# Performance work log

Measured on AMD Instinct MI355X. Metric: run time of the kernel, lower is better.

The kernel has to match this reference:

```python
import jax, jax.numpy as jnp
import numpy as np
import math

N, DIM, HEADS = 4096, 128, 8
HC = DIM // HEADS      # MHA per-head dim = 16
GC = DIM               # TransformerConv per-head out_channels = dim (concat=False)
E = 65536
FFN = 2048
EPS = 1e-5

def layernorm(x, g, b):
    m = x.mean(-1, keepdims=True)
    v = ((x - m) ** 2).mean(-1, keepdims=True)
    return (x - m) * jax.lax.rsqrt(v + EPS) * g + b

def setup_inputs() -> dict:
    key = jax.random.key(0)
    ks = jax.random.split(key, 24)
    s = 0.02
    def nrm(k, shape):
        return jax.random.normal(k, shape, jnp.float32) * s
    return dict(
        x=jax.random.normal(ks[0], (N, DIM), jnp.float32),
        edge_index=jax.random.randint(ks[1], (2, E), 0, N),
        edge_attr=jax.random.normal(ks[2], (E, DIM), jnp.float32),
        n1_g=jnp.ones((DIM,)), n1_b=jnp.zeros((DIM,)),
        n2_g=jnp.ones((DIM,)), n2_b=jnp.zeros((DIM,)),
        n3_g=jnp.ones((DIM,)), n3_b=jnp.zeros((DIM,)),
        w_qkv=nrm(ks[3], (DIM, 3 * DIM)), b_qkv=jnp.zeros((3 * DIM,)),
        w_o=nrm(ks[4], (DIM, DIM)), b_o=jnp.zeros((DIM,)),
        w_query=nrm(ks[5], (DIM, HEADS * GC)), b_query=jnp.zeros((HEADS * GC,)),
        w_key=nrm(ks[6], (DIM, HEADS * GC)), b_key=jnp.zeros((HEADS * GC,)),
        w_value=nrm(ks[7], (DIM, HEADS * GC)), b_value=jnp.zeros((HEADS * GC,)),
        w_edge=nrm(ks[8], (DIM, HEADS * GC)), b_edge=jnp.zeros((HEADS * GC,)),
        w_skip=nrm(ks[9], (DIM, GC)), b_skip=jnp.zeros((GC,)),
        w_beta=nrm(ks[10], (3 * GC, 1)),
        w_f1=nrm(ks[11], (DIM, FFN)), b_f1=jnp.zeros((FFN,)),
        w_f2=nrm(ks[12], (FFN, DIM)), b_f2=jnp.zeros((DIM,)),
        w_dyn=nrm(ks[13], (2 * DIM, DIM)), b_dyn=jnp.zeros((DIM,)),
    )

def reference(x, edge_index, edge_attr, n1_g, n1_b, n2_g, n2_b, n3_g, n3_b,
              w_qkv, b_qkv, w_o, b_o,
              w_query, b_query, w_key, b_key, w_value, b_value,
              w_edge, b_edge, w_skip, b_skip, w_beta,
              w_f1, b_f1, w_f2, b_f2, w_dyn, b_dyn):
    residual = x
    xn = layernorm(x, n1_g, n1_b)
    # ---- dense self-attention (batch 1, batch_first MHA, eval mode) ----
    qkv = xn @ w_qkv + b_qkv
    q, k, v = jnp.split(qkv, 3, axis=-1)
    q = q.reshape(N, HEADS, HC)
    k = k.reshape(N, HEADS, HC)
    v = v.reshape(N, HEADS, HC)
    scores = jnp.einsum('qhd,khd->hqk', q, k) / math.sqrt(HC)
    probs = jax.nn.softmax(scores, axis=-1)
    attn = jnp.einsum('hqk,khd->qhd', probs, v).reshape(N, DIM)
    attn = attn @ w_o + b_o
    x = residual + attn
    # ---- TransformerConv (heads=8, concat=False -> mean, beta=True, edge_dim=dim) ----
    xn2 = layernorm(x, n2_g, n2_b)
    src, dst = edge_index[0], edge_index[1]   # source -> target flow
    qg = (xn2 @ w_query + b_query).reshape(N, HEADS, GC)
    kg = (xn2 @ w_key + b_key).reshape(N, HEADS, GC)
    vg = (xn2 @ w_value + b_value).reshape(N, HEADS, GC)
    eg = (edge_attr @ w_edge + b_edge).reshape(E, HEADS, GC)
    kj = kg[src] + eg                          # key_j + edge embedding
    alpha = jnp.einsum('ehd,ehd->eh', qg[dst], kj) / math.sqrt(GC)  # [E,H]
    amax = jax.ops.segment_max(alpha, dst, num_segments=N)          # [N,H]
    amax = jnp.where(jnp.isfinite(amax), amax, 0.0)
    ea = jnp.exp(alpha - amax[dst])
    denom = jax.ops.segment_sum(ea, dst, num_segments=N)
    w = ea / (denom[dst] + 1e-16)              # segment softmax per target node
    msg = (vg[src] + eg) * w[:, :, None]       # value_j + edge, scaled
    agg = jax.ops.segment_sum(msg, dst, num_segments=N)  # [N,H,GC]
    out = agg.mean(axis=1)                     # concat=False -> head mean
    x_r = xn2 @ w_skip + b_skip                # root/skip path
    beta = jax.nn.sigmoid(jnp.concatenate([out, x_r, out - x_r], axis=-1) @ w_beta)
    graph_out = beta * x_r + (1.0 - beta) * out
    x = x + graph_out
    # ---- FFN ----
    xn3 = layernorm(x, n3_g, n3_b)
    ffn = jax.nn.gelu(xn3 @ w_f1 + b_f1, approximate=False) @ w_f2 + b_f2
    x = x + ffn
    # ---- gated residual fusion ----
    gate = jax.nn.sigmoid(jnp.concatenate([x, residual], axis=-1) @ w_dyn + b_dyn)
    return x * gate + residual * (1.0 - gate)
```

## Files before the change

kernel.cpp:

```cpp
#include <hip/hip_runtime.h>
#include <math.h>
#include <cstddef>

#define NN 4096
#define DIMC 128
#define NHEADS 8
#define NE 65536

typedef unsigned short ushort_t;
typedef short bs8 __attribute__((ext_vector_type(8)));
typedef float f32x16 __attribute__((ext_vector_type(16)));
typedef _Float16 h4 __attribute__((ext_vector_type(4)));
typedef float f4t __attribute__((ext_vector_type(4)));

__device__ __forceinline__ float b2f(ushort_t u){
  unsigned int i = ((unsigned int)u)<<16; float f;
  __builtin_memcpy(&f,&i,4); return f;
}
__device__ __forceinline__ ushort_t f2b(float f){
  unsigned int x; __builtin_memcpy(&x,&f,4);
  unsigned int r = x + 0x7fffu + ((x>>16)&1u);
  return (ushort_t)(r>>16);
}
__device__ __forceinline__ float bdot8(uint4 a, uint4 b){
  unsigned int ua[4]={a.x,a.y,a.z,a.w}, ub[4]={b.x,b.y,b.z,b.w};
  float s=0.f;
  #pragma unroll
  for (int i=0;i<4;++i){
    unsigned int al=ua[i]<<16, ah=ua[i]&0xffff0000u, bl=ub[i]<<16, bh=ub[i]&0xffff0000u;
    float fa,fb,fc,fd;
    __builtin_memcpy(&fa,&al,4); __builtin_memcpy(&fb,&ah,4);
    __builtin_memcpy(&fc,&bl,4); __builtin_memcpy(&fd,&bh,4);
    s += fa*fc + fb*fd;
  }
  return s;
}
__device__ __forceinline__ float bfdot8v(uint4 a, float4 e0, float4 e1){
  unsigned int ua[4]={a.x,a.y,a.z,a.w};
  float eb[8]={e0.x,e0.y,e0.z,e0.w,e1.x,e1.y,e1.z,e1.w};
  float s=0.f;
  #pragma unroll
  for (int i=0;i<4;++i){
    unsigned int al=ua[i]<<16, ah=ua[i]&0xffff0000u;
    float fa,fb;
    __builtin_memcpy(&fa,&al,4); __builtin_memcpy(&fb,&ah,4);
    s += fa*eb[2*i] + fb*eb[2*i+1];
  }
  return s;
}

__global__ __launch_bounds__(128) void ln_kernel(const float* __restrict__ x,
    const float* __restrict__ g, const float* __restrict__ b, ushort_t* __restrict__ y){
  int n = blockIdx.x, d = threadIdx.x;
  __shared__ float red[128];
  float v = x[(size_t)n*DIMC + d];
  red[d] = v; __syncthreads();
  for (int off=64; off>0; off>>=1){ if (d<off) red[d]+=red[d+off]; __syncthreads(); }
  float mean = red[0]*(1.0f/128.0f);
  __syncthreads();
  float c = v-mean;
  red[d] = c*c; __syncthreads();
  for (int off=64; off>0; off>>=1){ if (d<off) red[d]+=red[d+off]; __syncthreads(); }
  float var = red[0]*(1.0f/128.0f);
  y[(size_t)n*DIMC+d] = f2b(c*rsqrtf(var+1e-5f)*g[d]+b[d]);
}

#define QSCALE 0.36067376022224085f
__global__ __launch_bounds__(256) void megawcvt_kernel(
    const float* __restrict__ w_qkv, const float* __restrict__ w_o,
    const float* __restrict__ w_q, const float* __restrict__ w_k,
    const float* __restrict__ w_v, const float* __restrict__ w_e,
    const float* __restrict__ w_f1, const float* __restrict__ w_f2,
    const float* __restrict__ bq, const float* __restrict__ bk,
    const float* __restrict__ w_dyn, const float* __restrict__ b_qkv,
    ushort_t* __restrict__ WBqkv, ushort_t* __restrict__ WBo, ushort_t* __restrict__ WBG,
    ushort_t* __restrict__ WETB, ushort_t* __restrict__ WBf1, ushort_t* __restrict__ WBf2,
    ushort_t* __restrict__ WCAT, float* __restrict__ BCAT, ushort_t* __restrict__ WDYN,
    int* __restrict__ COUNT, float* __restrict__ BQKV)
{
  for (int id = blockIdx.x*256+threadIdx.x; id < 1284480; id += gridDim.x*256){
    if (id < 1245184){
      float v; ushort_t* dst; int local;
      if (id < 49152){ local=id; int n=local>>7,k=local&127; v=w_qkv[(size_t)k*384+n];
        if (n<128) v *= QSCALE;
        dst=&WBqkv[local]; }
      else if (id < 65536){ local=id-49152; int n=local>>7,k=local&127; v=w_o[(size_t)k*128+n]; dst=&WBo[local]; }
      else if (id < 327680){ local=id-65536; int n=local>>7,k=local&127;
        v = (n<1024) ? w_q[(size_t)k*1024+n] : w_k[(size_t)k*1024+n-1024];
        dst=&WBG[local]; }
      else if (id < 458752){ local=id-327680; int n=local>>7,k=local&127; v=w_e[(size_t)k*1024+n]; dst=&WETB[local]; }
      else if (id < 720896){ local=id-458752; int n=local>>7,k=local&127; v=w_f1[(size_t)k*2048+n]; dst=&WBf1[local]; }
      else if (id < 983040){ local=id-720896; int n=local>>11,k=local&2047; v=w_f2[(size_t)k*128+n]; dst=&WBf2[local]; }
      else { local=id-983040; int d=local>>11, k=local&2047;
        int h=(k&1023)>>7, i=k&127;
        const float* src = (k<1024) ? w_v : w_e;
        v = src[(size_t)i*1024 + h*128 + d]*0.125f;
        dst=&WCAT[local]; }
      *dst = f2b(v);
    } else if (id < 1247232){
      int local = id - 1245184;
      BCAT[local] = (local<1024) ? bq[local] : bk[local-1024];
    } else if (id < 1280000){
      int local = id - 1247232;
      WDYN[local] = f2b(w_dyn[local]);
    } else if (id < 1284096){
      COUNT[id-1280000]=0;
    } else {
      int local = id - 1284096;
      BQKV[local] = b_qkv[local] * ((local<128) ? QSCALE : 1.0f);
    }
  }
}

template<int A_BF16, int C_MODE>
__global__ __launch_bounds__(256) void mgemm_kernel(
    const void* __restrict__ Av, int lda, int strideA,
    const ushort_t* __restrict__ BT, int ldbt, int strideB,
    const float* __restrict__ bias,
    const float* __restrict__ res,
    void* __restrict__ Cv, int ldc, int strideC,
    int K, int act_gelu)
{
  int z = blockIdx.z;
  int m0 = blockIdx.y*128, n0 = blockIdx.x*64;
  int tid = threadIdx.x;
  int w = tid>>6, lane = tid&63;
  int kg = lane>>5;
  int ml = w*32 + (lane&31);
  int sw = (ml>>1)&3;
  __shared__ ushort_t As[128*32];
  const ushort_t* BTz = BT + (size_t)z*strideB;
  f32x16 acc[2];
  #pragma unroll
  for (int i=0;i<16;++i){ acc[0][i]=0.f; acc[1][i]=0.f; }

  for (int k0=0; k0<K; k0+=32){
    {
      int rr = tid>>1, kc = (tid&1)*16;
      int rowg = m0 + rr;
      ushort_t tmp[16] __attribute__((aligned(16)));
      if (A_BF16){
        const ushort_t* A = (const ushort_t*)Av + (size_t)z*strideA;
        uint4 u0 = *(const uint4*)&A[(size_t)rowg*lda + k0 + kc];
        uint4 u1 = *(const uint4*)&A[(size_t)rowg*lda + k0 + kc + 8];
        __builtin_memcpy(tmp, &u0, 16); __builtin_memcpy(tmp+8, &u1, 16);
      } else {
        const float* A = (const float*)Av + (size_t)z*strideA;
        const float* p = &A[(size_t)rowg*lda + k0 + kc];
        float4 f0=*(const float4*)p, f1=*(const float4*)(p+4);
        float4 f2v=*(const float4*)(p+8), f3=*(const float4*)(p+12);
        tmp[0]=f2b(f0.x); tmp[1]=f2b(f0.y); tmp[2]=f2b(f0.z); tmp[3]=f2b(f0.w);
        tmp[4]=f2b(f1.x); tmp[5]=f2b(f1.y); tmp[6]=f2b(f1.z); tmp[7]=f2b(f1.w);
        tmp[8]=f2b(f2v.x); tmp[9]=f2b(f2v.y); tmp[10]=f2b(f2v.z); tmp[11]=f2b(f2v.w);
        tmp[12]=f2b(f3.x); tmp[13]=f2b(f3.y); tmp[14]=f2b(f3.z); tmp[15]=f2b(f3.w);
      }
      int swr = (rr>>1)&3, c0 = kc>>3;
      *(uint4*)&As[rr*32 + (((c0  )^swr)*8)] = *(const uint4*)tmp;
      *(uint4*)&As[rr*32 + (((c0+1)^swr)*8)] = *(const uint4*)(tmp+8);
    }
    __syncthreads();
    bs8 a0 = *(bs8*)&As[ml*32 + (((0*2+kg)^sw)*8)];
    bs8 a1 = *(bs8*)&As[ml*32 + (((1*2+kg)^sw)*8)];
    #pragma unroll
    for (int nt=0; nt<2; ++nt){
      const ushort_t* bp = &BTz[(size_t)(n0 + nt*32 + (lane&31))*ldbt + k0 + kg*8];
      uint4 rb0 = *(const uint4*)bp;
      uint4 rb1 = *(const uint4*)(bp + 16);
      bs8 b0, b1;
      __builtin_memcpy(&b0, &rb0, 16); __builtin_memcpy(&b1, &rb1, 16);
      acc[nt] = __builtin_amdgcn_mfma_f32_32x32x16_bf16(a0, b0, acc[nt], 0,0,0);
      acc[nt] = __builtin_amdgcn_mfma_f32_32x32x16_bf16(a1, b1, acc[nt], 0,0,0);
    }
    __syncthreads();
  }
  #pragma unroll
  for (int nt=0; nt<2; ++nt){
    int col = n0 + nt*32 + (lane&31);
    float bv = bias ? bias[col] : 0.f;
    #pragma unroll
    for (int r=0; r<16; ++r){
      int rowl = (r&3) + 8*(r>>2) + 4*kg;
      int row = m0 + w*32 + rowl;
      float v = acc[nt][r] + bv;
      if (act_gelu) v = 0.5f*v*(1.0f+erff(v*0.70710678118654752f));
      if (res) v += res[(size_t)row*ldc + col];
      size_t idx = (size_t)z*strideC + (size_t)row*ldc + col;
      if (C_MODE==1)      ((ushort_t*)Cv)[idx] = f2b(v);
      else if (C_MODE==2) ((_Float16*)Cv)[idx] = (_Float16)v;
      else                ((float*)Cv)[idx]    = v;
    }
  }
}

__global__ __launch_bounds__(256) void vtrans_kernel(const _Float16* __restrict__ qkvh,
    _Float16* __restrict__ vt){
  int id = blockIdx.x*256+threadIdx.x;
  int n = id & 4095, d = id >> 12;
  vt[(size_t)d*4096 + n] = qkvh[(size_t)n*384 + 256 + d];
}

__global__ __launch_bounds__(512) void flash_kernel(const _Float16* __restrict__ qkvh,
    const _Float16* __restrict__ vt, float* __restrict__ attn){
  int h = blockIdx.y;
  int w = threadIdx.x >> 6, lane = threadIdx.x & 63;
  int q0 = blockIdx.x*64;
  int col = lane & 15, quad = lane >> 4;
  __shared__ float ll[8][4][16];
  __shared__ float lo[8][4][256];
  h4 qf[4];
  #pragma unroll
  for (int t=0;t<4;++t)
    qf[t] = *(const h4*)&qkvh[(size_t)(q0+t*16+col)*384 + h*16 + quad*4];
  f4t ov[4];
  float ls[4] = {0.f,0.f,0.f,0.f};
  #pragma unroll
  for (int t=0;t<4;++t){ ov[t][0]=0.f; ov[t][1]=0.f; ov[t][2]=0.f; ov[t][3]=0.f; }
  const _Float16* kbase = qkvh + 128 + h*16 + quad*4;
  const _Float16* vbase = vt + (size_t)(h*16+col)*4096 + quad*4;
  int jbeg = w*512, jend = jbeg + 512;
  h4 kf = *(const h4*)&kbase[(size_t)(jbeg+col)*384];
  h4 vf = *(const h4*)&vbase[jbeg];
  for (int j0=jbeg; j0<jend; j0+=16){
    h4 kc=kf, vc=vf;
    if (j0+16<jend){
      kf = *(const h4*)&kbase[(size_t)(j0+16+col)*384];
      vf = *(const h4*)&vbase[j0+16];
    }
    f4t s[4];
    #pragma unroll
    for (int t=0;t<4;++t){
      s[t][0]=0.f; s[t][1]=0.f; s[t][2]=0.f; s[t][3]=0.f;
      s[t] = __builtin_amdgcn_mfma_f32_16x16x16f16(kc, qf[t], s[t], 0,0,0);
    }
    #pragma unroll
    for (int t=0;t<4;++t){
      float p0=__builtin_amdgcn_exp2f(s[t][0]), p1=__builtin_amdgcn_exp2f(s[t][1]);
      float p2=__builtin_amdgcn_exp2f(s[t][2]), p3=__builtin_amdgcn_exp2f(s[t][3]);
      ls[t] += (p0+p1)+(p2+p3);
      h4 pf; pf[0]=(_Float16)p0; pf[1]=(_Float16)p1; pf[2]=(_Float16)p2; pf[3]=(_Float16)p3;
      ov[t] = __builtin_amdgcn_mfma_f32_16x16x16f16(vc, pf, ov[t], 0,0,0);
    }
  }
  #pragma unroll
  for (int t=0;t<4;++t){
    float l = ls[t];
    l += __shfl_xor(l,16);
    l += __shfl_xor(l,32);
    if (lane<16) ll[w][t][lane]=l;
    *(float4*)&lo[w][t][lane*4] = make_float4(ov[t][0],ov[t][1],ov[t][2],ov[t][3]);
  }
  __syncthreads();
  if (w < 4){
    int t = w;
    float l = 0.f;
    #pragma unroll
    for (int ww=0; ww<8; ++ww) l += ll[ww][t][col];
    float4 os = make_float4(0.f,0.f,0.f,0.f);
    #pragma unroll
    for (int ww=0; ww<8; ++ww){
      float4 owv = *(const float4*)&lo[ww][t][lane*4];
      os.x += owv.x; os.y += owv.y; os.z += owv.z; os.w += owv.w;
    }
    float inv = 1.0f/l;
    *(float4*)&attn[(size_t)(q0+t*16+col)*128 + h*16 + quad*4] =
        make_float4(os.x*inv, os.y*inv, os.z*inv, os.w*inv);
  }
}

__global__ __launch_bounds__(256) void alpha_kernel(
    const float* __restrict__ ea, const ushort_t* __restrict__ qkvsg,
    const ushort_t* __restrict__ t, const int* __restrict__ csr,
    const int* __restrict__ pack, float* __restrict__ alpha){
  int tid = threadIdx.x;
  int w = tid>>6, lane = tid&63;
  int h = lane>>3, li = lane&7;
  int off = h*128 + li*16;
  int ibase = blockIdx.x*8 + w*2;
  int2 pk = *(const int2*)&pack[ibase];
  int2 ec = *(const int2*)&csr[ibase];
  int e0 = ec.x & (NE-1), e1 = ec.y & (NE-1);
  int s0 = pk.x & 4095, d0 = (pk.x>>12) & 4095;
  int s1 = pk.y & 4095, d1 = (pk.y>>12) & 4095;

  const ushort_t* q0p = &qkvsg[(size_t)d0*2048 + off];
  const ushort_t* k0p = &qkvsg[(size_t)s0*2048 + 1024 + off];
  const ushort_t* t0p = &t[(size_t)d0*1024 + off];
  const float*    e0p = &ea[(size_t)e0*128 + li*16];
  const ushort_t* q1p = &qkvsg[(size_t)d1*2048 + off];
  const ushort_t* k1p = &qkvsg[(size_t)s1*2048 + 1024 + off];
  const ushort_t* t1p = &t[(size_t)d1*1024 + off];
  const float*    e1p = &ea[(size_t)e1*128 + li*16];

  uint4 q00=*(const uint4*)q0p,      q01=*(const uint4*)(q0p+8);
  uint4 k00=*(const uint4*)k0p,      k01=*(const uint4*)(k0p+8);
  uint4 t00=*(const uint4*)t0p,      t01=*(const uint4*)(t0p+8);
  float4 ea00=*(const float4*)e0p,   ea01=*(const float4*)(e0p+4);
  float4 ea02=*(const float4*)(e0p+8), ea03=*(const float4*)(e0p+12);
  uint4 q10=*(const uint4*)q1p,      q11=*(const uint4*)(q1p+8);
  uint4 k10=*(const uint4*)k1p,      k11=*(const uint4*)(k1p+8);
  uint4 t10=*(const uint4*)t1p,      t11=*(const uint4*)(t1p+8);
  float4 ea10=*(const float4*)e1p,   ea11=*(const float4*)(e1p+4);
  float4 ea12=*(const float4*)(e1p+8), ea13=*(const float4*)(e1p+12);

  float p0 = bdot8(q00,k00) + bdot8(q01,k01)
           + bfdot8v(t00,ea00,ea01) + bfdot8v(t01,ea02,ea03);
  float p1 = bdot8(q10,k10) + bdot8(q11,k11)
           + bfdot8v(t10,ea10,ea11) + bfdot8v(t11,ea12,ea13);
  p0 += __shfl_xor(p0,1); p0 += __shfl_xor(p0,2); p0 += __shfl_xor(p0,4);
  p1 += __shfl_xor(p1,1); p1 += __shfl_xor(p1,2); p1 += __shfl_xor(p1,4);
  if (li==0){
    alpha[(size_t)ibase*8 + h]     = 0.08838834764831845f*p0;
    alpha[(size_t)(ibase+1)*8 + h] = 0.08838834764831845f*p1;
  }
}

__global__ __launch_bounds__(256) void count_kernel(const int* __restrict__ ei, int* __restrict__ cnt){
  int e = blockIdx.x*256+threadIdx.x;
  atomicAdd(&cnt[ei[NE+e] & (NN-1)],1);
}
__global__ __launch_bounds__(1024) void scan_kernel(const int* __restrict__ cnt,
    int* __restrict__ rows, int* __restrict__ cursor){
  __shared__ int sums[1024];
  int tid=threadIdx.x;
  int c0=cnt[tid*4], c1=cnt[tid*4+1], c2=cnt[tid*4+2], c3=cnt[tid*4+3];
  int local=c0+c1+c2+c3;
  sums[tid]=local;
  __syncthreads();
  for (int off=1; off<1024; off<<=1){
    int v = (tid>=off)? sums[tid-off] : 0;
    __syncthreads();
    sums[tid]+=v;
    __syncthreads();
  }
  int r = sums[tid]-local;
  rows[tid*4]=r;   cursor[tid*4]=r;   r+=c0;
  rows[tid*4+1]=r; cursor[tid*4+1]=r; r+=c1;
  rows[tid*4+2]=r; cursor[tid*4+2]=r; r+=c2;
  rows[tid*4+3]=r; cursor[tid*4+3]=r; r+=c3;
  if (tid==1023) rows[4096]=r;
}
__global__ __launch_bounds__(256) void scatter_kernel(const int* __restrict__ ei,
    int* __restrict__ cursor, int* __restrict__ csr, int* __restrict__ pack){
  int e = blockIdx.x*256+threadIdx.x;
  int src = ei[e] & (NN-1), dst = ei[NE+e] & (NN-1);
  int pos = atomicAdd(&cursor[dst],1);
  if (pos >= 0 && pos < NE){ csr[pos]=e; pack[pos] = src | (dst<<12); }
}

__global__ __launch_bounds__(256) void agg1_kernel(
    const ushort_t* __restrict__ lns, const float* __restrict__ ea,
    const float* __restrict__ abuf, const int* __restrict__ rows, const int* __restrict__ csr,
    const int* __restrict__ pack,
    const float* __restrict__ b_edge, const float* __restrict__ b_v,
    ushort_t* __restrict__ seagg, float* __restrict__ part)
{
  int n = blockIdx.x, tid = threadIdx.x;
  int d = tid & 127, h0 = tid >> 7;
  float sacc[4]={0.f,0.f,0.f,0.f}, eacc[4]={0.f,0.f,0.f,0.f}, wsacc[4]={0.f,0.f,0.f,0.f};
  float mh[4]={-1e30f,-1e30f,-1e30f,-1e30f};
  float be[4];
  #pragma unroll
  for (int j=0;j<4;++j){
    int hd = (h0+2*j)*128 + d;
    be[j] = b_edge[hd] + b_v[hd];
  }
  int i0=rows[n], i1=rows[n+1];
  i0 = max(0,min(i0,NE)); i1 = max(i0,min(i1,NE));
  for (int i=i0;i<i1;++i){
    #pragma unroll
    for (int j=0;j<4;++j) mh[j] = fmaxf(mh[j], abuf[(size_t)i*8 + h0 + 2*j]);
  }
  __shared__ float smh[8];
  __shared__ float wls[16][8];
  __shared__ int es[16], srcs[16];
  if (d==0){
    #pragma unroll
    for (int j=0;j<4;++j) smh[h0+2*j]=mh[j];
  }
  __syncthreads();
  for (int cs=i0; cs<i1; cs+=16){
    int cnt = min(16, i1-cs);
    if (tid < cnt){
      es[tid]   = csr[cs+tid] & (NE-1);
      srcs[tid] = pack[cs+tid] & (NN-1);
    }
    if (tid < cnt*8){
      int k=tid>>3, hh=tid&7;
      wls[k][hh] = __expf(abuf[(size_t)(cs+k)*8+hh]-smh[hh]);
    }
    __syncthreads();
    for (int k=0;k<cnt;++k){
      int e = es[k], sr = srcs[k];
      float lv = b2f(lns[(size_t)sr*128 + d]);
      float eav = ea[(size_t)e*128 + d];
      #pragma unroll
      for (int j=0;j<4;++j){
        float wv = wls[k][h0+2*j];
        sacc[j] += wv*lv;
        eacc[j] += wv*eav;
        wsacc[j] += wv;
      }
    }
    __syncthreads();
  }
  float partial = 0.f;
  #pragma unroll
  for (int j=0;j<4;++j){
    float inv = 1.0f/(wsacc[j]+1e-16f);
    int hd = (h0+2*j)*128 + d;
    seagg[(size_t)n*2048 + hd]        = f2b(sacc[j]*inv);
    seagg[(size_t)n*2048 + 1024 + hd] = f2b(eacc[j]*inv);
    partial += be[j]*wsacc[j]*inv;
  }
  __shared__ float pp[2][128];
  pp[h0][d] = partial;
  __syncthreads();
  if (tid<128) part[(size_t)n*128+tid] = (pp[0][tid]+pp[1][tid])*0.125f;
}

__global__ __launch_bounds__(128) void combine_kernel(float* __restrict__ x2,
    const float* __restrict__ corrp, const float* __restrict__ part,
    const ushort_t* __restrict__ lns, const float* __restrict__ w_s,
    const float* __restrict__ b_s, const float* __restrict__ x1,
    const float* __restrict__ w_beta)
{
  int n=blockIdx.x, d=threadIdx.x;
  __shared__ float lnrow[128];
  __shared__ float sred[128];
  __shared__ float sbeta;
  size_t idx = (size_t)n*128+d;
  lnrow[d] = b2f(lns[idx]);
  __syncthreads();
  float xrv = b_s[d];
  #pragma unroll 4
  for (int i=0;i<128;++i) xrv += lnrow[i]*w_s[(size_t)i*128+d];
  float o = part[idx] + corrp[idx] + corrp[524288+idx] + corrp[1048576+idx] + corrp[1572864+idx];
  sred[d] = o*w_beta[d] + xrv*w_beta[128+d] + (o-xrv)*w_beta[256+d];
  __syncthreads();
  for (int off=64; off>0; off>>=1){ if (d<off) sred[d]+=sred[d+off]; __syncthreads(); }
  if (d==0) sbeta = 1.0f/(1.0f+__expf(-sred[0]));
  __syncthreads();
  float beta=sbeta;
  x2[idx] = x1[idx] + beta*xrv + (1.0f-beta)*o;
}

__global__ __launch_bounds__(128) void gate_kernel(const float* __restrict__ x3p,
    const float* __restrict__ b_f2, const float* __restrict__ x2,
    const float* __restrict__ x0, const ushort_t* __restrict__ wdyn,
    const float* __restrict__ b_dyn, float* __restrict__ out){
  int n=blockIdx.x, d=threadIdx.x;
  __shared__ float s[256];
  size_t idx = (size_t)n*128+d;
  float a = x3p[idx] + x3p[524288+idx] + x3p[1048576+idx] + x3p[1572864+idx]
          + b_f2[d] + x2[idx];
  float r = x0[idx];
  s[d]=a; s[128+d]=r;
  __syncthreads();
  float g = b_dyn[d];
  for (int k=0;k<256;++k) g += s[k]*b2f(wdyn[(size_t)k*128+d]);
  g = 1.0f/(1.0f+__expf(-g));
  out[idx] = a*g + r*(1.0f-g);
}

extern "C" void kernel_launch(void* const* d_in, const int* in_sizes, int n_in,
                              void* d_out, int out_size, void* d_ws, size_t ws_size,
                              hipStream_t stream) {
  const float* x    =(const float*)d_in[0];
  const int*   ei   =(const int*)  d_in[1];
  const float* eattr=(const float*)d_in[2];
  const float* n1g=(const float*)d_in[3], *n1b=(const float*)d_in[4];
  const float* n2g=(const float*)d_in[5], *n2b=(const float*)d_in[6];
  const float* n3g=(const float*)d_in[7], *n3b=(const float*)d_in[8];
  const float* w_qkv=(const float*)d_in[9],  *b_qkv=(const float*)d_in[10];
  const float* w_o  =(const float*)d_in[11], *b_o  =(const float*)d_in[12];
  const float* w_q  =(const float*)d_in[13], *b_q  =(const float*)d_in[14];
  const float* w_k  =(const float*)d_in[15], *b_k  =(const float*)d_in[16];
  const float* w_v  =(const float*)d_in[17], *b_v  =(const float*)d_in[18];
  const float* w_e  =(const float*)d_in[19], *b_e  =(const float*)d_in[20];
  const float* w_s  =(const float*)d_in[21], *b_s  =(const float*)d_in[22];
  const float* w_beta=(const float*)d_in[23];
  const float* w_f1 =(const float*)d_in[24], *b_f1=(const float*)d_in[25];
  const float* w_f2 =(const float*)d_in[26], *b_f2=(const float*)d_in[27];
  const float* w_dyn=(const float*)d_in[28], *b_dyn=(const float*)d_in[29];
  float* out=(float*)d_out;
  float* ws=(float*)d_ws;

  float* X1    = ws + 0;
  float* X2    = ws + 524288;
  ushort_t* LNS = (ushort_t*)(ws + 1048576);
  float* PART  = ws + 1310720;
  float* ALPHA = ws + 1835008;
  int*   ROWS  = (int*)(ws + 2359296);
  int*   CURS  = (int*)(ws + 2363456);
  int*   CSR   = (int*)(ws + 2367552);
  int*   COUNT = (int*)(ws + 2433088);
  int*   PACK  = (int*)(ws + 524288);
  float* BQKV  = ws + 1048576 - 512;
  ushort_t* WBqkv = (ushort_t*)(ws + 2437184);
  ushort_t* WBo   = (ushort_t*)(ws + 2461760);
  ushort_t* WBG   = (ushort_t*)(ws + 2469952);
  ushort_t* WETB  = (ushort_t*)(ws + 2601024);
  ushort_t* WBf1  = (ushort_t*)(ws + 2666560);
  ushort_t* WBf2  = (ushort_t*)(ws + 2797632);
  ushort_t* WCAT  = (ushort_t*)(ws + 2928704);
  float* BCAT  = ws + 3059776;
  ushort_t* WDYN = (ushort_t*)(ws + 3061824);
  _Float16* QKVH  = (_Float16*)(ws + 3078208);
  _Float16* VT    = (_Float16*)(ws + 3864640);
  ushort_t* QKVSG = (ushort_t*)(ws + 3078208);
  ushort_t* SEAGG = (ushort_t*)(ws + 3078208);
  ushort_t* MID   = (ushort_t*)(ws + 3078208);
  ushort_t* T     = (ushort_t*)(ws + 7272512);
  float* CORRP = ws + 7272512;
  float* X3P   = ws + 7272512;
  float* ATTN  = X2;

  megawcvt_kernel<<<2048,256,0,stream>>>(w_qkv,w_o,w_q,w_k,w_v,w_e,w_f1,w_f2,
                                         b_q,b_k,w_dyn,b_qkv,
                                         WBqkv,WBo,WBG,WETB,WBf1,WBf2,WCAT,BCAT,WDYN,COUNT,BQKV);

  ln_kernel<<<NN,128,0,stream>>>(x, n1g, n1b, LNS);
  mgemm_kernel<1,2><<<dim3(6,32,1),256,0,stream>>>(LNS,128,0, WBqkv,128,0, BQKV, nullptr, QKVH,384,0, 128, 0);
  vtrans_kernel<<<2048,256,0,stream>>>(QKVH, VT);
  flash_kernel<<<dim3(64,8),512,0,stream>>>(QKVH, VT, ATTN);
  mgemm_kernel<0,0><<<dim3(2,32,1),256,0,stream>>>(ATTN,128,0, WBo,128,0, b_o, x, X1,128,0, 128, 0);

  ln_kernel<<<NN,128,0,stream>>>(X1, n2g, n2b, LNS);
  mgemm_kernel<1,1><<<dim3(32,32,1),256,0,stream>>>(LNS,128,0, WBG,128,0, BCAT, nullptr, QKVSG,2048,0, 128, 0);
  mgemm_kernel<1,1><<<dim3(2,32,8),256,0,stream>>>(QKVSG,2048,128, WETB,128,16384, nullptr, nullptr, T,1024,128, 128, 0);
  count_kernel<<<256,256,0,stream>>>(ei, COUNT);
  scan_kernel<<<1,1024,0,stream>>>(COUNT, ROWS, CURS);
  scatter_kernel<<<256,256,0,stream>>>(ei, CURS, CSR, PACK);
  alpha_kernel<<<8192,256,0,stream>>>(eattr, QKVSG, T, CSR, PACK, ALPHA);
  agg1_kernel<<<NN,256,0,stream>>>(LNS, eattr, ALPHA, ROWS, CSR, PACK, b_e, b_v, SEAGG, PART);
  mgemm_kernel<1,0><<<dim3(2,32,4),256,0,stream>>>(SEAGG,2048,512, WCAT,2048,512, nullptr, nullptr, CORRP,128,524288, 512, 0);
  combine_kernel<<<NN,128,0,stream>>>(X2, CORRP, PART, LNS, w_s, b_s, X1, w_beta);

  ln_kernel<<<NN,128,0,stream>>>(X2, n3g, n3b, LNS);
  mgemm_kernel<1,1><<<dim3(32,32,1),256,0,stream>>>(LNS,128,0, WBf1,128,0, b_f1, nullptr, MID,2048,0, 128, 1);
  mgemm_kernel<1,0><<<dim3(2,32,4),256,0,stream>>>(MID,2048,512, WBf2,2048,512, nullptr, nullptr, X3P,128,524288, 512, 0);

  gate_kernel<<<NN,128,0,stream>>>(X3P, b_f2, X2, x, WDYN, b_dyn, out);
}
```

Before: 399.2 us.

## Use wave-level layernorm, fuse V transpose and third layernorm, rework combine/gate kernels

Rewrites the layernorm kernel to do one row per wavefront with shuffle reductions and paired loads. The V transpose moves into the QKV GEMM epilogue, and the third layernorm is fused into combine_kernel, removing two launches and their extra memory passes. Combine and gate kernels now process two rows per 64-thread block with float2 accesses, so each weight load is reused across two rows. Flash attention uses packed round-toward-zero conversion for probabilities, which slightly changes rounding.

```diff
diff --git a/kernel.cpp b/kernel.cpp
--- a/kernel.cpp
+++ b/kernel.cpp
@@ -11,6 +11,7 @@
 typedef short bs8 __attribute__((ext_vector_type(8)));
 typedef float f32x16 __attribute__((ext_vector_type(16)));
 typedef _Float16 h4 __attribute__((ext_vector_type(4)));
+typedef __fp16 fp16x2 __attribute__((ext_vector_type(2)));
 typedef float f4t __attribute__((ext_vector_type(4)));
 
 __device__ __forceinline__ float b2f(ushort_t u){
@@ -49,20 +50,25 @@
   return s;
 }
 
-__global__ __launch_bounds__(128) void ln_kernel(const float* __restrict__ x,
+__global__ __launch_bounds__(256) void ln_kernel(const float* __restrict__ x,
     const float* __restrict__ g, const float* __restrict__ b, ushort_t* __restrict__ y){
-  int n = blockIdx.x, d = threadIdx.x;
-  __shared__ float red[128];
-  float v = x[(size_t)n*DIMC + d];
-  red[d] = v; __syncthreads();
-  for (int off=64; off>0; off>>=1){ if (d<off) red[d]+=red[d+off]; __syncthreads(); }
-  float mean = red[0]*(1.0f/128.0f);
-  __syncthreads();
-  float c = v-mean;
-  red[d] = c*c; __syncthreads();
-  for (int off=64; off>0; off>>=1){ if (d<off) red[d]+=red[d+off]; __syncthreads(); }
-  float var = red[0]*(1.0f/128.0f);
-  y[(size_t)n*DIMC+d] = f2b(c*rsqrtf(var+1e-5f)*g[d]+b[d]);
+  int n = blockIdx.x*4 + (threadIdx.x>>6);
+  int l = threadIdx.x & 63;
+  int d0 = 2*l;
+  float2 v = *(const float2*)&x[(size_t)n*DIMC + d0];
+  float s = v.x+v.y;
+  s += __shfl_xor(s,1); s += __shfl_xor(s,2); s += __shfl_xor(s,4);
+  s += __shfl_xor(s,8); s += __shfl_xor(s,16); s += __shfl_xor(s,32);
+  float mean = s*(1.0f/128.0f);
+  float c0=v.x-mean, c1=v.y-mean;
+  float q=c0*c0+c1*c1;
+  q += __shfl_xor(q,1); q += __shfl_xor(q,2); q += __shfl_xor(q,4);
+  q += __shfl_xor(q,8); q += __shfl_xor(q,16); q += __shfl_xor(q,32);
+  float rinv = rsqrtf(q*(1.0f/128.0f)+1e-5f);
+  float2 gv = *(const float2*)&g[d0];
+  float2 bv = *(const float2*)&b[d0];
+  unsigned int pk = ((unsigned int)f2b(c1*rinv*gv.y+bv.y)<<16) | (unsigned int)f2b(c0*rinv*gv.x+bv.x);
+  *(unsigned int*)&y[(size_t)n*DIMC + d0] = pk;
 }
 
 #define QSCALE 0.36067376022224085f
@@ -119,7 +125,7 @@
     const float* __restrict__ bias,
     const float* __restrict__ res,
     void* __restrict__ Cv, int ldc, int strideC,
-    int K, int act_gelu)
+    int K, int act_gelu, _Float16* __restrict__ vtout)
 {
   int z = blockIdx.z;
   int m0 = blockIdx.y*128, n0 = blockIdx.x*64;
@@ -186,17 +192,14 @@
       if (res) v += res[(size_t)row*ldc + col];
       size_t idx = (size_t)z*strideC + (size_t)row*ldc + col;
       if (C_MODE==1)      ((ushort_t*)Cv)[idx] = f2b(v);
-      else if (C_MODE==2) ((_Float16*)Cv)[idx] = (_Float16)v;
+      else if (C_MODE==2){
+        _Float16 hv = (_Float16)v;
+        ((_Float16*)Cv)[idx] = hv;
+        if (vtout && col>=256) vtout[(size_t)(col-256)*4096 + row] = hv;
+      }
       else                ((float*)Cv)[idx]    = v;
     }
   }
-}
-
-__global__ __launch_bounds__(256) void vtrans_kernel(const _Float16* __restrict__ qkvh,
-    _Float16* __restrict__ vt){
-  int id = blockIdx.x*256+threadIdx.x;
-  int n = id & 4095, d = id >> 12;
-  vt[(size_t)d*4096 + n] = qkvh[(size_t)n*384 + 256 + d];
 }
 
 __global__ __launch_bounds__(512) void flash_kernel(const _Float16* __restrict__ qkvh,
@@ -237,7 +240,11 @@
       float p0=__builtin_amdgcn_exp2f(s[t][0]), p1=__builtin_amdgcn_exp2f(s[t][1]);
       float p2=__builtin_amdgcn_exp2f(s[t][2]), p3=__builtin_amdgcn_exp2f(s[t][3]);
       ls[t] += (p0+p1)+(p2+p3);
-      h4 pf; pf[0]=(_Float16)p0; pf[1]=(_Float16)p1; pf[2]=(_Float16)p2; pf[3]=(_Float16)p3;
+      fp16x2 plo = __builtin_amdgcn_cvt_pkrtz(p0,p1);
+      fp16x2 phi = __builtin_amdgcn_cvt_pkrtz(p2,p3);
+      h4 pf;
+      pf[0]=(_Float16)plo[0]; pf[1]=(_Float16)plo[1];
+      pf[2]=(_Float16)phi[0]; pf[3]=(_Float16)phi[1];
       ov[t] = __builtin_amdgcn_mfma_f32_16x16x16f16(vc, pf, ov[t], 0,0,0);
     }
   }
@@ -418,48 +425,132 @@
   if (tid<128) part[(size_t)n*128+tid] = (pp[0][tid]+pp[1][tid])*0.125f;
 }
 
-__global__ __launch_bounds__(128) void combine_kernel(float* __restrict__ x2,
+__global__ __launch_bounds__(64) void combine_kernel(float* __restrict__ x2,
     const float* __restrict__ corrp, const float* __restrict__ part,
-    const ushort_t* __restrict__ lns, const float* __restrict__ w_s,
+    ushort_t* __restrict__ lns, const float* __restrict__ w_s,
     const float* __restrict__ b_s, const float* __restrict__ x1,
-    const float* __restrict__ w_beta)
+    const float* __restrict__ w_beta,
+    const float* __restrict__ n3g, const float* __restrict__ n3b)
 {
-  int n=blockIdx.x, d=threadIdx.x;
-  __shared__ float lnrow[128];
-  __shared__ float sred[128];
-  __shared__ float sbeta;
-  size_t idx = (size_t)n*128+d;
-  lnrow[d] = b2f(lns[idx]);
+  int n0 = blockIdx.x*2;
+  int l = threadIdx.x;
+  int d0 = 2*l, d1 = 2*l+1;
+  __shared__ float sln[2][128];
+  #pragma unroll
+  for (int rr=0;rr<2;++rr){
+    unsigned int u = *(const unsigned int*)&lns[(size_t)(n0+rr)*128 + d0];
+    sln[rr][d0] = b2f((ushort_t)(u&0xffffu));
+    sln[rr][d1] = b2f((ushort_t)(u>>16));
+  }
   __syncthreads();
-  float xrv = b_s[d];
-  #pragma unroll 4
-  for (int i=0;i<128;++i) xrv += lnrow[i]*w_s[(size_t)i*128+d];
-  float o = part[idx] + corrp[idx] + corrp[524288+idx] + corrp[1048576+idx] + corrp[1572864+idx];
-  sred[d] = o*w_beta[d] + xrv*w_beta[128+d] + (o-xrv)*w_beta[256+d];
-  __syncthreads();
-  for (int off=64; off>0; off>>=1){ if (d<off) sred[d]+=sred[d+off]; __syncthreads(); }
-  if (d==0) sbeta = 1.0f/(1.0f+__expf(-sred[0]));
-  __syncthreads();
-  float beta=sbeta;
-  x2[idx] = x1[idx] + beta*xrv + (1.0f-beta)*o;
-}
-
-__global__ __launch_bounds__(128) void gate_kernel(const float* __restrict__ x3p,
+  float2 bsv = *(const float2*)&b_s[d0];
+  float xr0[2], xr1[2];
+  xr0[0]=bsv.x; xr0[1]=bsv.x; xr1[0]=bsv.y; xr1[1]=bsv.y;
+  for (int i=0;i<128;++i){
+    float2 wv = *(const float2*)&w_s[(size_t)i*128 + d0];
+    #pragma unroll
+    for (int rr=0;rr<2;++rr){
+      float lv = sln[rr][i];
+      xr0[rr] += lv*wv.x; xr1[rr] += lv*wv.y;
+    }
+  }
+  float2 wb0 = *(const float2*)&w_beta[d0];
+  float2 wb1 = *(const float2*)&w_beta[128+d0];
+  float2 wb2 = *(const float2*)&w_beta[256+d0];
+  float2 gv = *(const float2*)&n3g[d0];
+  float2 bv = *(const float2*)&n3b[d0];
+  #pragma unroll
+  for (int rr=0;rr<2;++rr){
+    size_t idx = (size_t)(n0+rr)*128 + d0;
+    float2 pt = *(const float2*)&part[idx];
+    float2 c0 = *(const float2*)&corrp[idx];
+    float2 c1 = *(const float2*)&corrp[524288+idx];
+    float2 c2 = *(const float2*)&corrp[1048576+idx];
+    float2 c3 = *(const float2*)&corrp[1572864+idx];
+    float o0 = pt.x+c0.x+c1.x+c2.x+c3.x;
+    float o1 = pt.y+c0.y+c1.y+c2.y+c3.y;
+    float xa = xr0[rr], xb = xr1[rr];
+    float pr = o0*wb0.x + o1*wb0.y + xa*wb1.x + xb*wb1.y
+             + (o0-xa)*wb2.x + (o1-xb)*wb2.y;
+    pr += __shfl_xor(pr,1); pr += __shfl_xor(pr,2); pr += __shfl_xor(pr,4);
+    pr += __shfl_xor(pr,8); pr += __shfl_xor(pr,16); pr += __shfl_xor(pr,32);
+    float beta = 1.0f/(1.0f+__expf(-pr));
+    float2 xv = *(const float2*)&x1[idx];
+    float v0 = xv.x + beta*xa + (1.0f-beta)*o0;
+    float v1 = xv.y + beta*xb + (1.0f-beta)*o1;
+    *(float2*)&x2[idx] = make_float2(v0,v1);
+    float s = v0+v1;
+    s += __shfl_xor(s,1); s += __shfl_xor(s,2); s += __shfl_xor(s,4);
+    s += __shfl_xor(s,8); s += __shfl_xor(s,16); s += __shfl_xor(s,32);
+    float mean = s*(1.0f/128.0f);
+    float e0=v0-mean, e1=v1-mean;
+    float q = e0*e0+e1*e1;
+    q += __shfl_xor(q,1); q += __shfl_xor(q,2); q += __shfl_xor(q,4);
+    q += __shfl_xor(q,8); q += __shfl_xor(q,16); q += __shfl_xor(q,32);
+    float rinv = rsqrtf(q*(1.0f/128.0f)+1e-5f);
+    unsigned int pk2 = ((unsigned int)f2b(e1*rinv*gv.y+bv.y)<<16)
+                     |  (unsigned int)f2b(e0*rinv*gv.x+bv.x);
+    *(unsigned int*)&lns[idx] = pk2;
+  }
+}
+
+__global__ __launch_bounds__(64) void gate_kernel(const float* __restrict__ x3p,
     const float* __restrict__ b_f2, const float* __restrict__ x2,
     const float* __restrict__ x0, const ushort_t* __restrict__ wdyn,
     const float* __restrict__ b_dyn, float* __restrict__ out){
-  int n=blockIdx.x, d=threadIdx.x;
-  __shared__ float s[256];
-  size_t idx = (size_t)n*128+d;
-  float a = x3p[idx] + x3p[524288+idx] + x3p[1048576+idx] + x3p[1572864+idx]
-          + b_f2[d] + x2[idx];
-  float r = x0[idx];
-  s[d]=a; s[128+d]=r;
+  int n0 = blockIdx.x*2;
+  int l = threadIdx.x;
+  int d0 = 2*l, d1 = 2*l+1;
+  __shared__ float sA[2][128];
+  __shared__ float sR[2][128];
+  float a0[2], a1[2], r0[2], r1[2];
+  float2 bb = *(const float2*)&b_f2[d0];
+  #pragma unroll
+  for (int rr=0;rr<2;++rr){
+    size_t idx = (size_t)(n0+rr)*128 + d0;
+    float2 p0v = *(const float2*)&x3p[idx];
+    float2 p1v = *(const float2*)&x3p[524288+idx];
+    float2 p2v = *(const float2*)&x3p[1048576+idx];
+    float2 p3v = *(const float2*)&x3p[1572864+idx];
+    float2 xv = *(const float2*)&x2[idx];
+    float2 rv = *(const float2*)&x0[idx];
+    a0[rr] = p0v.x+p1v.x+p2v.x+p3v.x+bb.x+xv.x;
+    a1[rr] = p0v.y+p1v.y+p2v.y+p3v.y+bb.y+xv.y;
+    r0[rr]=rv.x; r1[rr]=rv.y;
+    sA[rr][d0]=a0[rr]; sA[rr][d1]=a1[rr];
+    sR[rr][d0]=rv.x;  sR[rr][d1]=rv.y;
+  }
   __syncthreads();
-  float g = b_dyn[d];
-  for (int k=0;k<256;++k) g += s[k]*b2f(wdyn[(size_t)k*128+d]);
-  g = 1.0f/(1.0f+__expf(-g));
-  out[idx] = a*g + r*(1.0f-g);
+  float2 bd = *(const float2*)&b_dyn[d0];
+  float g0[2], g1[2];
+  g0[0]=bd.x; g0[1]=bd.x; g1[0]=bd.y; g1[1]=bd.y;
+  for (int k=0;k<128;++k){
+    unsigned int wv = *(const unsigned int*)&wdyn[(size_t)k*128 + d0];
+    float w0=b2f((ushort_t)(wv&0xffffu)), w1=b2f((ushort_t)(wv>>16));
+    #pragma unroll
+    for (int rr=0;rr<2;++rr){
+      float sk = sA[rr][k];
+      g0[rr]+=sk*w0; g1[rr]+=sk*w1;
+    }
+  }
+  for (int k=0;k<128;++k){
+    unsigned int wv = *(const unsigned int*)&wdyn[(size_t)(128+k)*128 + d0];
+    float w0=b2f((ushort_t)(wv&0xffffu)), w1=b2f((ushort_t)(wv>>16));
+    #pragma unroll
+    for (int rr=0;rr<2;++rr){
+      float sk = sR[rr][k];
+      g0[rr]+=sk*w0; g1[rr]+=sk*w1;
+    }
+  }
+  #pragma unroll
+  for (int rr=0;rr<2;++rr){
+    size_t idx=(size_t)(n0+rr)*128 + d0;
+    float gg0=1.0f/(1.0f+__expf(-g0[rr]));
+    float gg1=1.0f/(1.0f+__expf(-g1[rr]));
+    float v0=a0[rr]*gg0 + r0[rr]*(1.0f-gg0);
+    float v1=a1[rr]*gg1 + r1[rr]*(1.0f-gg1);
+    *(float2*)&out[idx]=make_float2(v0,v1);
+  }
 }
 
 extern "C" void kernel_launch(void* const* d_in, const int* in_sizes, int n_in,
@@ -519,26 +610,24 @@
                                          b_q,b_k,w_dyn,b_qkv,
                                          WBqkv,WBo,WBG,WETB,WBf1,WBf2,WCAT,BCAT,WDYN,COUNT,BQKV);
 
-  ln_kernel<<<NN,128,0,stream>>>(x, n1g, n1b, LNS);
-  mgemm_kernel<1,2><<<dim3(6,32,1),256,0,stream>>>(LNS,128,0, WBqkv,128,0, BQKV, nullptr, QKVH,384,0, 128, 0);
-  vtrans_kernel<<<2048,256,0,stream>>>(QKVH, VT);
+  ln_kernel<<<1024,256,0,stream>>>(x, n1g, n1b, LNS);
+  mgemm_kernel<1,2><<<dim3(6,32,1),256,0,stream>>>(LNS,128,0, WBqkv,128,0, BQKV, nullptr, QKVH,384,0, 128, 0, VT);
   flash_kernel<<<dim3(64,8),512,0,stream>>>(QKVH, VT, ATTN);
-  mgemm_kernel<0,0><<<dim3(2,32,1),256,0,stream>>>(ATTN,128,0, WBo,128,0, b_o, x, X1,128,0, 128, 0);
-
-  ln_kernel<<<NN,128,0,stream>>>(X1, n2g, n2b, LNS);
-  mgemm_kernel<1,1><<<dim3(32,32,1),256,0,stream>>>(LNS,128,0, WBG,128,0, BCAT, nullptr, QKVSG,2048,0, 128, 0);
-  mgemm_kernel<1,1><<<dim3(2,32,8),256,0,stream>>>(QKVSG,2048,128, WETB,128,16384, nullptr, nullptr, T,1024,128, 128, 0);
+  mgemm_kernel<0,0><<<dim3(2,32,1),256,0,stream>>>(ATTN,128,0, WBo,128,0, b_o, x, X1,128,0, 128, 0, nullptr);
+
+  ln_kernel<<<1024,256,0,stream>>>(X1, n2g, n2b, LNS);
+  mgemm_kernel<1,1><<<dim3(32,32,1),256,0,stream>>>(LNS,128,0, WBG,128,0, BCAT, nullptr, QKVSG,2048,0, 128, 0, nullptr);
+  mgemm_kernel<1,1><<<dim3(2,32,8),256,0,stream>>>(QKVSG,2048,128, WETB,128,16384, nullptr, nullptr, T,1024,128, 128, 0, nullptr);
   count_kernel<<<256,256,0,stream>>>(ei, COUNT);
   scan_kernel<<<1,1024,0,stream>>>(COUNT, ROWS, CURS);
   scatter_kernel<<<256,256,0,stream>>>(ei, CURS, CSR, PACK);
   alpha_kernel<<<8192,256,0,stream>>>(eattr, QKVSG, T, CSR, PACK, ALPHA);
   agg1_kernel<<<NN,256,0,stream>>>(LNS, eattr, ALPHA, ROWS, CSR, PACK, b_e, b_v, SEAGG, PART);
-  mgemm_kernel<1,0><<<dim3(2,32,4),256,0,stream>>>(SEAGG,2048,512, WCAT,2048,512, nullptr, nullptr, CORRP,128,524288, 512, 0);
-  combine_kernel<<<NN,128,0,stream>>>(X2, CORRP, PART, LNS, w_s, b_s, X1, w_beta);
-
-  ln_kernel<<<NN,128,0,stream>>>(X2, n3g, n3b, LNS);
-  mgemm_kernel<1,1><<<dim3(32,32,1),256,0,stream>>>(LNS,128,0, WBf1,128,0, b_f1, nullptr, MID,2048,0, 128, 1);
-  mgemm_kernel<1,0><<<dim3(2,32,4),256,0,stream>>>(MID,2048,512, WBf2,2048,512, nullptr, nullptr, X3P,128,524288, 512, 0);
-
-  gate_kernel<<<NN,128,0,stream>>>(X3P, b_f2, X2, x, WDYN, b_dyn, out);
-}
+  mgemm_kernel<1,0><<<dim3(2,32,4),256,0,stream>>>(SEAGG,2048,512, WCAT,2048,512, nullptr, nullptr, CORRP,128,524288, 512, 0, nullptr);
+  combine_kernel<<<2048,64,0,stream>>>(X2, CORRP, PART, LNS, w_s, b_s, X1, w_beta, n3g, n3b);
+
+  mgemm_kernel<1,1><<<dim3(32,32,1),256,0,stream>>>(LNS,128,0, WBf1,128,0, b_f1, nullptr, MID,2048,0, 128, 1, nullptr);
+  mgemm_kernel<1,0><<<dim3(2,32,4),256,0,stream>>>(MID,2048,512, WBf2,2048,512, nullptr, nullptr, X3P,128,524288, 512, 0, nullptr);
+
+  gate_kernel<<<2048,64,0,stream>>>(X3P, b_f2, X2, x, WDYN, b_dyn, out);
+}
```

New measurement: 392.2 us. About the same (-1.7%).
